# Optimization experiments

Measured on AMD Instinct MI355X. Metric: run time of the kernel, lower is better.

## Reference

```python
import jax, jax.numpy as jnp
import numpy as np

N_NODES, N_EDGES, N_GRAPHS = 20000, 320000, 16
F_NODE, F_EDGE, F_GLOB = 64, 32, 16


def seg_mean(x, idx, num):
    # segment average; segments with zero members yield zeros
    s = jax.ops.segment_sum(x, idx, num_segments=num)
    c = jax.ops.segment_sum(jnp.ones((x.shape[0], 1), x.dtype), idx, num_segments=num)
    return s / jnp.maximum(c, 1.0)


def setup_inputs() -> dict:
    key = jax.random.key(0)
    ks = jax.random.split(key, 24)
    s = 0.05
    inp = {
        'node_feats': jax.random.normal(ks[0], (N_NODES, F_NODE), jnp.float32),
        'edge_feats': jax.random.normal(ks[1], (N_EDGES, F_EDGE), jnp.float32),
        'globals_': jax.random.normal(ks[2], (N_GRAPHS, F_GLOB), jnp.float32),
        'We1': jax.random.normal(ks[3], (256, F_EDGE), jnp.float32) * s,
        'be1': jnp.zeros((256,), jnp.float32),
        'Wn1': jax.random.normal(ks[4], (256, F_NODE), jnp.float32) * s,
        'Win1': jax.random.normal(ks[5], (256, 256), jnp.float32) * s,
        'bn1': jnp.zeros((256,), jnp.float32),
        'We2': jax.random.normal(ks[6], (128, 256), jnp.float32) * s,
        'Wg2': jax.random.normal(ks[7], (128, F_GLOB), jnp.float32) * s,
        'be2': jnp.zeros((128,), jnp.float32),
        'Wn2': jax.random.normal(ks[8], (128, 256), jnp.float32) * s,
        'Win2': jax.random.normal(ks[9], (128, 128), jnp.float32) * s,
        'Wng2': jax.random.normal(ks[10], (128, F_GLOB), jnp.float32) * s,
        'bn2': jnp.zeros((128,), jnp.float32),
        'Wgn': jax.random.normal(ks[11], (128, 128), jnp.float32) * s,
        'Wge': jax.random.normal(ks[12], (128, 128), jnp.float32) * s,
        'Wgg': jax.random.normal(ks[13], (128, F_GLOB), jnp.float32) * s,
        'bg': jnp.zeros((128,), jnp.float32),
        'receivers': jax.random.randint(ks[14], (N_EDGES,), 0, N_NODES, jnp.int32),
        'node_graph': jnp.sort(jax.random.randint(ks[15], (N_NODES,), 0, N_GRAPHS, jnp.int32)),
    }
    return inp


def reference(node_feats, edge_feats, globals_, We1, be1, Wn1, Win1, bn1,
              We2, Wg2, be2, Wn2, Win2, Wng2, bn2, Wgn, Wge, Wgg, bg,
              receivers, node_graph):
    N = node_feats.shape[0]
    B = globals_.shape[0]
    edge_graph = node_graph[receivers]  # graph id of each edge [E]

    # edge1 + relu: e -> 256
    e1 = jax.nn.relu(edge_feats @ We1.T + be1)  # [E,256]
    # node1 + relu: node + avg incoming edges -> 256
    agg1 = seg_mean(e1, receivers, N)  # [N,256]
    n1 = jax.nn.relu(node_feats @ Wn1.T + agg1 @ Win1.T + bn1)  # [N,256]
    # edge2 + relu: edge + broadcast globals -> 128
    e2 = jax.nn.relu(e1 @ We2.T + globals_[edge_graph] @ Wg2.T + be2)  # [E,128]
    # node2 + relu: node + avg incoming edges + broadcast globals -> 128
    agg2 = seg_mean(e2, receivers, N)  # [N,128]
    n2 = jax.nn.relu(n1 @ Wn2.T + agg2 @ Win2.T + globals_[node_graph] @ Wng2.T + bn2)  # [N,128]
    # global: avg nodes + avg edges per graph + globals -> output
    node_avg = seg_mean(n2, node_graph, B)  # [B,128]
    edge_avg = seg_mean(e2, edge_graph, B)  # [B,128]
    out = node_avg @ Wgn.T + edge_avg @ Wge.T + globals_ @ Wgg.T + bg  # [B,128]
    return out
```

## Files before the change

### kernel.cpp

```cpp
#include <hip/hip_runtime.h>
#include <hip/hip_bf16.h>

#define N_NODES 20000
#define N_EDGES 320000
#define NG 16

using bf16 = __hip_bfloat16;
typedef __attribute__((ext_vector_type(8))) short short8v;
typedef __attribute__((ext_vector_type(4))) short short4v;
typedef __attribute__((ext_vector_type(4))) float f32x4;

static __device__ __forceinline__ short f2bs(float f) {
  bf16 h = __float2bfloat16(f);
  union { bf16 b; short s; } u;
  u.b = h;
  return u.s;
}
static __device__ __forceinline__ float bs2f(short s) {
  union { short s; bf16 b; } u;
  u.s = s;
  return __bfloat162float(u.b);
}

__global__ __launch_bounds__(256) void k_prep(
    const float* __restrict__ globals_, const float* __restrict__ Wg2,
    const float* __restrict__ Wng2, const float* __restrict__ Wgg,
    const float* __restrict__ bg, float* __restrict__ g2e,
    float* __restrict__ g2n, float* __restrict__ gg,
    const float* __restrict__ We1, const float* __restrict__ Wn1,
    const float* __restrict__ Win1, const float* __restrict__ We2,
    const float* __restrict__ Wn2, const float* __restrict__ Win2,
    bf16* __restrict__ Wb_e1, bf16* __restrict__ Wb_n1,
    bf16* __restrict__ Wb_e2, bf16* __restrict__ Wb_n2,
    const float* __restrict__ nf, bf16* __restrict__ nfb) {
  int idx = blockIdx.x * 256 + threadIdx.x;
  if (idx < 6144) {
    int arr = idx >> 11;
    int rem = idx & 2047;
    int g = rem >> 7, c = rem & 127;
    const float* W = arr == 0 ? Wg2 : (arr == 1 ? Wng2 : Wgg);
    float acc = (arr == 2) ? bg[c] : 0.f;
#pragma unroll
    for (int k = 0; k < 16; ++k) acc += globals_[g * 16 + k] * W[c * 16 + k];
    float* o = arr == 0 ? g2e : (arr == 1 ? g2n : gg);
    o[rem] = acc;
    return;
  }
  idx -= 6144;
  if (idx < 172032) {
    int i = idx;
    float v;
    bf16* dst;
    int di;
    if (i < 8192) {
      v = We1[i]; dst = Wb_e1; di = i;
    } else if (i < 90112) {
      int j = i - 8192, r = j / 320, c = j % 320;
      v = c < 64 ? Wn1[r * 64 + c] : Win1[r * 256 + (c - 64)];
      dst = Wb_n1; di = j;
    } else if (i < 122880) {
      int j = i - 90112;
      int n = j >> 8, p = j & 255;
      int k = ((p & 15) << 4) | (p >> 4);
      v = We2[n * 256 + k];
      dst = Wb_e2; di = j;
    } else {
      int j = i - 122880, r = j / 384, c = j % 384;
      if (c < 256) {
        int k = ((c & 15) << 4) | (c >> 4);
        v = Wn2[r * 256 + k];
      } else {
        v = Win2[r * 128 + (c - 256)];
      }
      dst = Wb_n2; di = j;
    }
    dst[di] = __float2bfloat16(v);
    return;
  }
  idx -= 172032;
  if (idx < 320000) {
    int n = idx >> 4, q = idx & 15;
    float4 v = *(const float4*)(nf + (size_t)n * 64 + q * 4);
    short4v o = {f2bs(v.x), f2bs(v.y), f2bs(v.z), f2bs(v.w)};
    *(short4v*)((short*)nfb + (size_t)n * 64 + q * 4) = o;
  }
}

__global__ __launch_bounds__(256) void k_counts(
    const int* __restrict__ recv, const int* __restrict__ node_graph,
    int* __restrict__ cnt_node, int* __restrict__ node_cnt_g,
    int* __restrict__ edge_cnt_g) {
  __shared__ int le[NG], ln[NG];
  int tid = threadIdx.x;
  if (tid < NG) { le[tid] = 0; ln[tid] = 0; }
  __syncthreads();
  int idx = blockIdx.x * 256 + tid;
  if (idx < N_EDGES) {
    int r = recv[idx];
    atomicAdd(&cnt_node[r], 1);
    atomicAdd(&le[node_graph[r]], 1);
  } else if (idx < N_EDGES + N_NODES) {
    int n = idx - N_EDGES;
    atomicAdd(&ln[node_graph[n]], 1);
  }
  __syncthreads();
  if (tid < NG && le[tid]) atomicAdd(&edge_cnt_g[tid], le[tid]);
  if (tid >= NG && tid < 2 * NG && ln[tid - NG]) atomicAdd(&node_cnt_g[tid - NG], ln[tid - NG]);
}

__global__ __launch_bounds__(256) void k_scan(const int* __restrict__ cnt,
                                              int* __restrict__ offset,
                                              int* __restrict__ cursor) {
  __shared__ int wsum[4];
  __shared__ int carry_s;
  int tid = threadIdx.x, lane = tid & 63, wv = tid >> 6;
  if (tid == 0) carry_s = 0;
  __syncthreads();
  for (int base = 0; base < N_NODES; base += 1024) {
    int idx = base + tid * 4;
    int v[4];
    int s = 0;
#pragma unroll
    for (int i = 0; i < 4; ++i) {
      v[i] = (idx + i < N_NODES) ? cnt[idx + i] : 0;
      s += v[i];
    }
    int ps = s;
#pragma unroll
    for (int d = 1; d < 64; d <<= 1) {
      int t = __shfl_up(ps, d, 64);
      if (lane >= d) ps += t;
    }
    if (lane == 63) wsum[wv] = ps;
    __syncthreads();
    int wbase = carry_s;
    for (int w2 = 0; w2 < wv; ++w2) wbase += wsum[w2];
    int run = wbase + ps - s;
#pragma unroll
    for (int i = 0; i < 4; ++i) {
      if (idx + i < N_NODES) {
        offset[idx + i] = run;
        cursor[idx + i] = 0;
      }
      run += v[i];
    }
    __syncthreads();
    if (tid == 0) carry_s += wsum[0] + wsum[1] + wsum[2] + wsum[3];
    __syncthreads();
  }
  if (tid == 0) offset[N_NODES] = carry_s;
}

__global__ __launch_bounds__(256) void k_scatter(
    const int* __restrict__ recv, const int* __restrict__ offset,
    int* __restrict__ cursor, int* __restrict__ pos2edge,
    int* __restrict__ pos2node) {
  int e = blockIdx.x * 256 + threadIdx.x;
  if (e >= N_EDGES) return;
  int n = recv[e];
  int slot = atomicAdd(&cursor[n], 1);
  int pos = offset[n] + slot;
  pos2edge[pos] = e;
  pos2node[pos] = n;
}

__global__ __launch_bounds__(256, 4) void k_edge(
    const float* __restrict__ edge_feats, const bf16* __restrict__ We1b,
    const bf16* __restrict__ We2b, const float* __restrict__ be1,
    const float* __restrict__ be2, const float* __restrict__ g2e,
    const int* __restrict__ pos2edge, const int* __restrict__ pos2node,
    const int* __restrict__ node_graph, const int* __restrict__ offset,
    float* __restrict__ agg1f, float* __restrict__ agg2f) {
  __shared__ __align__(16) short t16[64 * 264];
  __shared__ int rownode_s[64];
  __shared__ int rowgid_s[64];
  char* tb = (char*)t16;
  const int tid = threadIdx.x;
  const int wave = tid >> 6, lane = tid & 63;
  const int l15 = lane & 15, grp = lane >> 4;
  const int p0 = blockIdx.x * 64;
  const int base = wave * 16;

  if (tid < 64) {
    int rn = pos2node[p0 + tid];
    rownode_s[tid] = rn;
    rowgid_s[tid] = node_graph[rn];
  }
  const int n0w = tid >> 3, cgw = tid & 7;
  short8v wreg[4];
#pragma unroll
  for (int s = 0; s < 4; ++s)
    wreg[s] = *(const short8v*)((const short*)We2b + (size_t)(n0w + s * 32) * 256 + cgw * 8);
#pragma unroll
  for (int s = 0; s < 4; ++s) {
    int slot = tid + s * 256;
    int n = slot >> 2, cg = slot & 3;
    short8v w8 = *(const short8v*)((const short*)We1b + n * 32 + cg * 8);
    *(short8v*)(tb + n * 64 + ((cg * 16) ^ (((n >> 1) & 3) << 4))) = w8;
  }
  int e = pos2edge[p0 + base + l15];
  const float* efrow = edge_feats + (size_t)e * 32 + grp * 8;
  float4 af0 = *(const float4*)(efrow);
  float4 af1 = *(const float4*)(efrow + 4);
  short8v a1;
  a1[0] = f2bs(af0.x); a1[1] = f2bs(af0.y); a1[2] = f2bs(af0.z); a1[3] = f2bs(af0.w);
  a1[4] = f2bs(af1.x); a1[5] = f2bs(af1.y); a1[6] = f2bs(af1.z); a1[7] = f2bs(af1.w);
  __syncthreads();

  f32x4 acc1[16] = {};
#pragma unroll
  for (int nf = 0; nf < 16; ++nf) {
    int n = nf * 16 + l15;
    short8v b8 = *(const short8v*)(tb + n * 64 + ((grp * 16) ^ (((n >> 1) & 3) << 4)));
    acc1[nf] = __builtin_amdgcn_mfma_f32_16x16x32_bf16(a1, b8, acc1[nf], 0, 0, 0);
  }
#pragma unroll
  for (int nf = 0; nf < 16; ++nf) {
    float bv = be1[nf * 16 + l15];
#pragma unroll
    for (int i = 0; i < 4; ++i) {
      float v = acc1[nf][i] + bv;
      acc1[nf][i] = v > 0.f ? v : 0.f;
    }
  }
  __syncthreads();

#pragma unroll
  for (int i = 0; i < 4; ++i) {
    int row = base + grp * 4 + i;
    short8v lo, hi;
#pragma unroll
    for (int q = 0; q < 8; ++q) {
      lo[q] = f2bs(acc1[q][i]);
      hi[q] = f2bs(acc1[q + 8][i]);
    }
    *(short8v*)&t16[row * 264 + l15 * 16] = lo;
    *(short8v*)&t16[row * 264 + l15 * 16 + 8] = hi;
  }
  __syncthreads();

  bool bnd = (lane == 63) || (rownode_s[lane + 1] != rownode_s[lane]);
  unsigned long long fmask = __ballot(bnd);
  unsigned long long amask = 0;
  {
    unsigned long long lsb = fmask & (~fmask + 1ull);
    if (offset[rownode_s[0]] < p0) amask |= lsb;
    if (offset[rownode_s[63] + 1] > p0 + 64) amask |= 1ull << 63;
  }

  short8v a2[8];
  const short* myrow = &t16[(base + l15) * 264];
#pragma unroll
  for (int s = 0; s < 8; ++s)
    a2[s] = *(const short8v*)(myrow + s * 32 + grp * 8);

  {
    int col = ((tid & 15) << 4) | (tid >> 4);
    float run = 0.f;
#pragma unroll
    for (int rb = 0; rb < 64; rb += 16) {
      float v[16];
#pragma unroll
      for (int i = 0; i < 16; ++i) v[i] = bs2f(t16[(rb + i) * 264 + tid]);
#pragma unroll
      for (int i = 0; i < 16; ++i) {
        run += v[i];
        int r = rb + i;
        if ((fmask >> r) & 1) {
          float* dst = &agg1f[(size_t)rownode_s[r] * 256 + col];
          if ((amask >> r) & 1) atomicAdd(dst, run);
          else *dst = run;
          run = 0.f;
        }
      }
    }
  }
  __syncthreads();

#pragma unroll
  for (int s = 0; s < 4; ++s) {
    int n = n0w + s * 32;
    *(short8v*)(tb + n * 128 + ((cgw * 16) ^ ((n & 7) << 4))) = wreg[s];
  }
#pragma unroll
  for (int s = 0; s < 4; ++s)
    wreg[s] = *(const short8v*)((const short*)We2b + (size_t)(n0w + s * 32) * 256 + 64 + cgw * 8);
  __syncthreads();

  f32x4 acc2[8] = {};
#pragma unroll
  for (int c = 0; c < 4; ++c) {
    const int bufo = (c & 1) ? 16384 : 0;
    if (c < 3) {
      const int nbufo = ((c + 1) & 1) ? 16384 : 0;
#pragma unroll
      for (int s = 0; s < 4; ++s) {
        int n = n0w + s * 32;
        *(short8v*)(tb + nbufo + n * 128 + ((cgw * 16) ^ ((n & 7) << 4))) = wreg[s];
      }
      if (c < 2) {
#pragma unroll
        for (int s = 0; s < 4; ++s)
          wreg[s] = *(const short8v*)((const short*)We2b +
                                      (size_t)(n0w + s * 32) * 256 + (c + 2) * 64 + cgw * 8);
      }
    }
#pragma unroll
    for (int kki = 0; kki < 2; ++kki) {
#pragma unroll
      for (int nf = 0; nf < 8; ++nf) {
        int n = nf * 16 + l15;
        short8v b8 = *(const short8v*)(tb + bufo + n * 128 +
                                       (((kki * 64) + grp * 16) ^ ((n & 7) << 4)));
        acc2[nf] = __builtin_amdgcn_mfma_f32_16x16x32_bf16(a2[c * 2 + kki], b8,
                                                           acc2[nf], 0, 0, 0);
      }
    }
    if (c < 3) __syncthreads();
  }

  int gidr[4];
#pragma unroll
  for (int i = 0; i < 4; ++i) gidr[i] = rowgid_s[base + grp * 4 + i];
#pragma unroll
  for (int nf = 0; nf < 8; ++nf) {
    int col = nf * 16 + l15;
    float bv = be2[col];
#pragma unroll
    for (int i = 0; i < 4; ++i) {
      float v = acc2[nf][i] + bv + g2e[gidr[i] * 128 + col];
      acc2[nf][i] = v > 0.f ? v : 0.f;
    }
  }
  __syncthreads();

  float* tf32 = (float*)t16;
#pragma unroll
  for (int i = 0; i < 4; ++i) {
    int row = base + grp * 4 + i;
    float4 lo = {acc2[0][i], acc2[1][i], acc2[2][i], acc2[3][i]};
    float4 hi = {acc2[4][i], acc2[5][i], acc2[6][i], acc2[7][i]};
    *(float4*)&tf32[row * 132 + l15 * 8] = lo;
    *(float4*)&tf32[row * 132 + l15 * 8 + 4] = hi;
  }
  __syncthreads();

  if (tid < 128) {
    int col = ((tid & 7) << 4) | (tid >> 3);
    float run = 0.f;
#pragma unroll
    for (int rb = 0; rb < 64; rb += 16) {
      float v[16];
#pragma unroll
      for (int i = 0; i < 16; ++i) v[i] = tf32[(rb + i) * 132 + tid];
#pragma unroll
      for (int i = 0; i < 16; ++i) {
        run += v[i];
        int r = rb + i;
        if ((fmask >> r) & 1) {
          float* dst = &agg2f[(size_t)rownode_s[r] * 128 + col];
          if ((amask >> r) & 1) atomicAdd(dst, run);
          else *dst = run;
          run = 0.f;
        }
      }
    }
  }
}

__global__ __launch_bounds__(256, 2) void k_node(
    const bf16* __restrict__ nfb, const float* __restrict__ agg1f,
    const float* __restrict__ agg2f, const int* __restrict__ offset,
    const bf16* __restrict__ Wn1b, const bf16* __restrict__ Wn2b,
    const float* __restrict__ bn1, const float* __restrict__ bn2,
    const float* __restrict__ g2n, const int* __restrict__ node_graph,
    float* __restrict__ node_sum, float* __restrict__ edge_sum) {
  __shared__ __align__(16) char smem_w[32768];
  __shared__ __align__(16) short t16[64 * 264];
  __shared__ int rowgid_s[64];
  const int tid = threadIdx.x;
  const int wave = tid >> 6, lane = tid & 63;
  const int l15 = lane & 15, grp = lane >> 4;
  const int r0 = blockIdx.x * 64;
  const int base = wave * 16;
  const int n0w = tid >> 3, cgw = tid & 7;

  if (tid < 64) {
    int n = r0 + tid;
    rowgid_s[tid] = node_graph[n < N_NODES ? n : N_NODES - 1];
  }
  long arow = r0 + base + l15;
  if (arow >= N_NODES) arow = N_NODES - 1;
  int dg = offset[arow + 1] - offset[arow];
  const float inv = 1.f / (float)(dg > 1 ? dg : 1);

  short8v a1all[10];
#pragma unroll
  for (int kki = 0; kki < 2; ++kki)
    a1all[kki] = *(const short8v*)((const short*)nfb + (size_t)arow * 64 + kki * 32 + grp * 8);
#pragma unroll
  for (int c = 1; c < 5; ++c) {
#pragma unroll
    for (int kki = 0; kki < 2; ++kki) {
      int k = c * 64 + kki * 32 + grp * 8;
      const float* p = agg1f + (size_t)arow * 256 + (k - 64);
      float4 f0 = *(const float4*)p;
      float4 f1 = *(const float4*)(p + 4);
      short8v t;
      t[0] = f2bs(f0.x * inv); t[1] = f2bs(f0.y * inv);
      t[2] = f2bs(f0.z * inv); t[3] = f2bs(f0.w * inv);
      t[4] = f2bs(f1.x * inv); t[5] = f2bs(f1.y * inv);
      t[6] = f2bs(f1.z * inv); t[7] = f2bs(f1.w * inv);
      a1all[c * 2 + kki] = t;
    }
  }

  short8v w1x[8], w1y[8];
#pragma unroll
  for (int s = 0; s < 8; ++s)
    w1x[s] = *(const short8v*)((const short*)Wn1b + (size_t)(n0w + s * 32) * 320 + cgw * 8);
#pragma unroll
  for (int s = 0; s < 8; ++s)
    w1y[s] = *(const short8v*)((const short*)Wn1b + (size_t)(n0w + s * 32) * 320 + 64 + cgw * 8);
  f32x4 acc1[16] = {};
#pragma unroll
  for (int c = 0; c < 5; ++c) {
    if (c > 0) __syncthreads();
#pragma unroll
    for (int s = 0; s < 8; ++s) {
      int n = n0w + s * 32;
      *(short8v*)(smem_w + n * 128 + ((cgw * 16) ^ ((n & 7) << 4))) =
          (c & 1) ? w1y[s] : w1x[s];
    }
    if (c + 2 < 5) {
#pragma unroll
      for (int s = 0; s < 8; ++s) {
        short8v t = *(const short8v*)((const short*)Wn1b +
                                      (size_t)(n0w + s * 32) * 320 + (c + 2) * 64 + cgw * 8);
        if (c & 1) w1y[s] = t;
        else w1x[s] = t;
      }
    }
    __syncthreads();
#pragma unroll
    for (int kki = 0; kki < 2; ++kki) {
#pragma unroll
      for (int nf = 0; nf < 16; ++nf) {
        int wrow = nf * 16 + l15;
        short8v b8 = *(const short8v*)(smem_w + wrow * 128 +
                                       (((kki * 64) + grp * 16) ^ ((wrow & 7) << 4)));
        acc1[nf] = __builtin_amdgcn_mfma_f32_16x16x32_bf16(a1all[c * 2 + kki], b8,
                                                           acc1[nf], 0, 0, 0);
      }
    }
  }

#pragma unroll
  for (int nf = 0; nf < 16; ++nf) {
    float bv = bn1[nf * 16 + l15];
#pragma unroll
    for (int i = 0; i < 4; ++i) {
      float v = acc1[nf][i] + bv;
      acc1[nf][i] = v > 0.f ? v : 0.f;
    }
  }
#pragma unroll
  for (int i = 0; i < 4; ++i) {
    int row = base + grp * 4 + i;
    short8v lo, hi;
#pragma unroll
    for (int q = 0; q < 8; ++q) {
      lo[q] = f2bs(acc1[q][i]);
      hi[q] = f2bs(acc1[q + 8][i]);
    }
    *(short8v*)&t16[row * 264 + l15 * 16] = lo;
    *(short8v*)&t16[row * 264 + l15 * 16 + 8] = hi;
  }
  short8v a2all[12];
  const short* myrow = &t16[(base + l15) * 264];
#pragma unroll
  for (int s = 0; s < 8; ++s)
    a2all[s] = *(const short8v*)(myrow + s * 32 + grp * 8);
#pragma unroll
  for (int c = 4; c < 6; ++c) {
#pragma unroll
    for (int kki = 0; kki < 2; ++kki) {
      int k = (c - 4) * 64 + kki * 32 + grp * 8;
      const float* p = agg2f + (size_t)arow * 128 + k;
      float4 f0 = *(const float4*)p;
      float4 f1 = *(const float4*)(p + 4);
      short8v t;
      t[0] = f2bs(f0.x * inv); t[1] = f2bs(f0.y * inv);
      t[2] = f2bs(f0.z * inv); t[3] = f2bs(f0.w * inv);
      t[4] = f2bs(f1.x * inv); t[5] = f2bs(f1.y * inv);
      t[6] = f2bs(f1.z * inv); t[7] = f2bs(f1.w * inv);
      a2all[c * 2 + kki] = t;
    }
  }
  short8v w2r[24];
#pragma unroll
  for (int c = 0; c < 6; ++c)
#pragma unroll
    for (int s = 0; s < 4; ++s)
      w2r[c * 4 + s] = *(const short8v*)((const short*)Wn2b +
                                         (size_t)(n0w + s * 32) * 384 + c * 64 + cgw * 8);

  f32x4 acc2[8] = {};
#pragma unroll
  for (int c = 0; c < 6; ++c) {
    __syncthreads();
#pragma unroll
    for (int s = 0; s < 4; ++s) {
      int n = n0w + s * 32;
      *(short8v*)(smem_w + n * 128 + ((cgw * 16) ^ ((n & 7) << 4))) = w2r[c * 4 + s];
    }
    __syncthreads();
#pragma unroll
    for (int kki = 0; kki < 2; ++kki) {
#pragma unroll
      for (int nf = 0; nf < 8; ++nf) {
        int wrow = nf * 16 + l15;
        short8v b8 = *(const short8v*)(smem_w + wrow * 128 +
                                       (((kki * 64) + grp * 16) ^ ((wrow & 7) << 4)));
        acc2[nf] = __builtin_amdgcn_mfma_f32_16x16x32_bf16(a2all[c * 2 + kki], b8,
                                                           acc2[nf], 0, 0, 0);
      }
    }
  }

  float* tf32 = (float*)t16;
  int gidr[4];
#pragma unroll
  for (int i = 0; i < 4; ++i) gidr[i] = rowgid_s[base + grp * 4 + i];
#pragma unroll
  for (int nf = 0; nf < 8; ++nf) {
    int col = nf * 16 + l15;
    float bv = bn2[col];
#pragma unroll
    for (int i = 0; i < 4; ++i) {
      float v = acc2[nf][i] + bv + g2n[gidr[i] * 128 + col];
      acc2[nf][i] = v > 0.f ? v : 0.f;
    }
  }
#pragma unroll
  for (int i = 0; i < 4; ++i) {
    int row = base + grp * 4 + i;
    float4 lo = {acc2[0][i], acc2[1][i], acc2[2][i], acc2[3][i]};
    float4 hi = {acc2[4][i], acc2[5][i], acc2[6][i], acc2[7][i]};
    *(float4*)&tf32[row * 132 + l15 * 8] = lo;
    *(float4*)&tf32[row * 132 + l15 * 8 + 4] = hi;
  }
  __syncthreads();

  bool gb = (lane == 63) || (rowgid_s[lane + 1] != rowgid_s[lane]);
  unsigned long long gmask = __ballot(gb);
  if (tid < 128) {
    int col = ((tid & 7) << 4) | (tid >> 3);
    float rn_ = 0.f, re_ = 0.f;
#pragma unroll
    for (int rb = 0; rb < 64; rb += 16) {
      float vn[16], ve[16];
#pragma unroll
      for (int i = 0; i < 16; ++i) {
        int r = rb + i;
        long row = (long)r0 + r;
        bool ok = row < N_NODES;
        vn[i] = ok ? tf32[r * 132 + tid] : 0.f;
        ve[i] = ok ? agg2f[(size_t)row * 128 + col] : 0.f;
      }
#pragma unroll
      for (int i = 0; i < 16; ++i) {
        int r = rb + i;
        rn_ += vn[i];
        re_ += ve[i];
        if ((gmask >> r) & 1) {
          int g = rowgid_s[r];
          atomicAdd(&node_sum[g * 128 + col], rn_);
          atomicAdd(&edge_sum[g * 128 + col], re_);
          rn_ = 0.f;
          re_ = 0.f;
        }
      }
    }
  }
}

__global__ __launch_bounds__(128) void k_final(
    const float* __restrict__ node_sum, const float* __restrict__ edge_sum,
    const int* __restrict__ node_cnt_g, const int* __restrict__ edge_cnt_g,
    const float* __restrict__ Wgn, const float* __restrict__ Wge,
    const float* __restrict__ gg, float* __restrict__ out) {
  __shared__ float navg[128], eavg[128];
  const int g = blockIdx.x, c = threadIdx.x;
  int nc = node_cnt_g[g];
  nc = nc > 1 ? nc : 1;
  int ec = edge_cnt_g[g];
  ec = ec > 1 ? ec : 1;
  navg[c] = node_sum[g * 128 + c] / (float)nc;
  eavg[c] = edge_sum[g * 128 + c] / (float)ec;
  __syncthreads();
  float acc = gg[g * 128 + c];
#pragma unroll 4
  for (int k = 0; k < 128; ++k)
    acc += navg[k] * Wgn[c * 128 + k] + eavg[k] * Wge[c * 128 + k];
  out[g * 128 + c] = acc;
}

extern "C" void kernel_launch(void* const* d_in, const int* in_sizes, int n_in,
                              void* d_out, int out_size, void* d_ws, size_t ws_size,
                              hipStream_t stream) {
  const float* node_feats = (const float*)d_in[0];
  const float* edge_feats = (const float*)d_in[1];
  const float* globals_ = (const float*)d_in[2];
  const float* We1 = (const float*)d_in[3];
  const float* be1 = (const float*)d_in[4];
  const float* Wn1 = (const float*)d_in[5];
  const float* Win1 = (const float*)d_in[6];
  const float* bn1 = (const float*)d_in[7];
  const float* We2 = (const float*)d_in[8];
  const float* Wg2 = (const float*)d_in[9];
  const float* be2 = (const float*)d_in[10];
  const float* Wn2 = (const float*)d_in[11];
  const float* Win2 = (const float*)d_in[12];
  const float* Wng2 = (const float*)d_in[13];
  const float* bn2 = (const float*)d_in[14];
  const float* Wgn = (const float*)d_in[15];
  const float* Wge = (const float*)d_in[16];
  const float* Wgg = (const float*)d_in[17];
  const float* bg = (const float*)d_in[18];
  const int* receivers = (const int*)d_in[19];
  const int* node_graph = (const int*)d_in[20];
  float* out = (float*)d_out;

  char* ws = (char*)d_ws;
  size_t off = 0;
  auto alloc = [&](size_t bytes) {
    size_t o = off;
    off += (bytes + 255) & ~(size_t)255;
    return o;
  };
  const int NP = 20032;
  int* cnt_node = (int*)(ws + alloc((size_t)N_NODES * 4));
  int* node_cnt_g = (int*)(ws + alloc(NG * 4));
  int* edge_cnt_g = (int*)(ws + alloc(NG * 4));
  float* node_sum = (float*)(ws + alloc(NG * 128 * 4));
  float* edge_sum = (float*)(ws + alloc(NG * 128 * 4));
  float* agg1f = (float*)(ws + alloc((size_t)N_NODES * 256 * 4));
  float* agg2f = (float*)(ws + alloc((size_t)N_NODES * 128 * 4));
  size_t zero_bytes = off;
  int* offset = (int*)(ws + alloc((size_t)(N_NODES + 1) * 4));
  int* cursor = (int*)(ws + alloc((size_t)N_NODES * 4));
  int* pos2edge = (int*)(ws + alloc((size_t)N_EDGES * 4));
  int* pos2node = (int*)(ws + alloc((size_t)N_EDGES * 4));
  float* g2e = (float*)(ws + alloc(NG * 128 * 4));
  float* g2n = (float*)(ws + alloc(NG * 128 * 4));
  float* gg = (float*)(ws + alloc(NG * 128 * 4));
  bf16* Wb_e1 = (bf16*)(ws + alloc(8192 * 2));
  bf16* Wb_n1 = (bf16*)(ws + alloc(81920 * 2));
  bf16* Wb_e2 = (bf16*)(ws + alloc(32768 * 2));
  bf16* Wb_n2 = (bf16*)(ws + alloc(49152 * 2));
  bf16* nfb = (bf16*)(ws + alloc((size_t)NP * 64 * 2));
  (void)ws_size;

  hipMemsetAsync(d_ws, 0, zero_bytes, stream);
  k_prep<<<1946, 256, 0, stream>>>(globals_, Wg2, Wng2, Wgg, bg, g2e, g2n, gg,
                                   We1, Wn1, Win1, We2, Wn2, Win2, Wb_e1,
                                   Wb_n1, Wb_e2, Wb_n2, node_feats, nfb);
  k_counts<<<(N_EDGES + N_NODES + 255) / 256, 256, 0, stream>>>(
      receivers, node_graph, cnt_node, node_cnt_g, edge_cnt_g);
  k_scan<<<1, 256, 0, stream>>>(cnt_node, offset, cursor);
  k_scatter<<<(N_EDGES + 255) / 256, 256, 0, stream>>>(receivers, offset,
                                                       cursor, pos2edge,
                                                       pos2node);
  k_edge<<<N_EDGES / 64, 256, 0, stream>>>(edge_feats, Wb_e1, Wb_e2, be1, be2,
                                           g2e, pos2edge, pos2node, node_graph,
                                           offset, agg1f, agg2f);
  k_node<<<NP / 64, 256, 0, stream>>>(nfb, agg1f, agg2f, offset, Wb_n1, Wb_n2,
                                      bn1, bn2, g2n, node_graph, node_sum,
                                      edge_sum);
  k_final<<<NG, 128, 0, stream>>>(node_sum, edge_sum, node_cnt_g, edge_cnt_g,
                                  Wgn, Wge, gg, out);
}
```

Baseline: 195.7 us.

## Make edge kernel persistent over five tiles with prefetch of next tile

The edge kernel now launches 1000 blocks that each process five 64-edge tiles in a loop instead of one tile per block. While the current tile is being reduced into agg1f, each block prefetches the next tile's edge features, node ids and graph ids, and it also reloads the first We2 chunk for the next iteration. The aim is to hide global load latency and amortize per-block setup. The cost is fewer blocks in flight (1000 blocks on a large GPU), extra register pressure, and the We1 tile being restaged into shared memory on every iteration.

```diff
diff --git a/kernel.cpp b/kernel.cpp
--- a/kernel.cpp
+++ b/kernel.cpp
@@ -172,199 +172,243 @@
     const int* __restrict__ node_graph, const int* __restrict__ offset,
     float* __restrict__ agg1f, float* __restrict__ agg2f) {
   __shared__ __align__(16) short t16[64 * 264];
-  __shared__ int rownode_s[64];
-  __shared__ int rowgid_s[64];
+  __shared__ int rownode_s[2][64];
+  __shared__ int rowgid_s[2][64];
   char* tb = (char*)t16;
   const int tid = threadIdx.x;
   const int wave = tid >> 6, lane = tid & 63;
   const int l15 = lane & 15, grp = lane >> 4;
-  const int p0 = blockIdx.x * 64;
   const int base = wave * 16;
-
-  if (tid < 64) {
-    int rn = pos2node[p0 + tid];
-    rownode_s[tid] = rn;
-    rowgid_s[tid] = node_graph[rn];
-  }
   const int n0w = tid >> 3, cgw = tid & 7;
+
+  int rn_next = 0, rg_next = 0;
+  short8v a1_next;
   short8v wreg[4];
-#pragma unroll
-  for (int s = 0; s < 4; ++s)
-    wreg[s] = *(const short8v*)((const short*)We2b + (size_t)(n0w + s * 32) * 256 + cgw * 8);
-#pragma unroll
-  for (int s = 0; s < 4; ++s) {
-    int slot = tid + s * 256;
-    int n = slot >> 2, cg = slot & 3;
-    short8v w8 = *(const short8v*)((const short*)We1b + n * 32 + cg * 8);
-    *(short8v*)(tb + n * 64 + ((cg * 16) ^ (((n >> 1) & 3) << 4))) = w8;
-  }
-  int e = pos2edge[p0 + base + l15];
-  const float* efrow = edge_feats + (size_t)e * 32 + grp * 8;
-  float4 af0 = *(const float4*)(efrow);
-  float4 af1 = *(const float4*)(efrow + 4);
-  short8v a1;
-  a1[0] = f2bs(af0.x); a1[1] = f2bs(af0.y); a1[2] = f2bs(af0.z); a1[3] = f2bs(af0.w);
-  a1[4] = f2bs(af1.x); a1[5] = f2bs(af1.y); a1[6] = f2bs(af1.z); a1[7] = f2bs(af1.w);
-  __syncthreads();
-
-  f32x4 acc1[16] = {};
-#pragma unroll
-  for (int nf = 0; nf < 16; ++nf) {
-    int n = nf * 16 + l15;
-    short8v b8 = *(const short8v*)(tb + n * 64 + ((grp * 16) ^ (((n >> 1) & 3) << 4)));
-    acc1[nf] = __builtin_amdgcn_mfma_f32_16x16x32_bf16(a1, b8, acc1[nf], 0, 0, 0);
-  }
-#pragma unroll
-  for (int nf = 0; nf < 16; ++nf) {
-    float bv = be1[nf * 16 + l15];
+  {
+    const int tile0 = blockIdx.x * 5;
+    if (tid < 64) {
+      rn_next = pos2node[tile0 * 64 + tid];
+      rg_next = node_graph[rn_next];
+    }
+    int e0 = pos2edge[tile0 * 64 + base + l15];
+    const float* er = edge_feats + (size_t)e0 * 32 + grp * 8;
+    float4 a = *(const float4*)er;
+    float4 b = *(const float4*)(er + 4);
+    a1_next[0] = f2bs(a.x); a1_next[1] = f2bs(a.y);
+    a1_next[2] = f2bs(a.z); a1_next[3] = f2bs(a.w);
+    a1_next[4] = f2bs(b.x); a1_next[5] = f2bs(b.y);
+    a1_next[6] = f2bs(b.z); a1_next[7] = f2bs(b.w);
+#pragma unroll
+    for (int s = 0; s < 4; ++s)
+      wreg[s] = *(const short8v*)((const short*)We2b + (size_t)(n0w + s * 32) * 256 + cgw * 8);
+  }
+
+#pragma unroll 1
+  for (int t = 0; t < 5; ++t) {
+    const int tile = blockIdx.x * 5 + t;
+    const int p0 = tile * 64;
+    const int pr = t & 1;
+    __syncthreads();
+    if (tid < 64) {
+      rownode_s[pr][tid] = rn_next;
+      rowgid_s[pr][tid] = rg_next;
+    }
+#pragma unroll
+    for (int s = 0; s < 4; ++s) {
+      int slot = tid + s * 256;
+      int n = slot >> 2, cg = slot & 3;
+      short8v w8 = *(const short8v*)((const short*)We1b + n * 32 + cg * 8);
+      *(short8v*)(tb + n * 64 + ((cg * 16) ^ (((n >> 1) & 3) << 4))) = w8;
+    }
+    short8v a1 = a1_next;
+    __syncthreads();
+
+    f32x4 acc1[16] = {};
+#pragma unroll
+    for (int nf = 0; nf < 16; ++nf) {
+      int n = nf * 16 + l15;
+      short8v b8 = *(const short8v*)(tb + n * 64 + ((grp * 16) ^ (((n >> 1) & 3) << 4)));
+      acc1[nf] = __builtin_amdgcn_mfma_f32_16x16x32_bf16(a1, b8, acc1[nf], 0, 0, 0);
+    }
+#pragma unroll
+    for (int nf = 0; nf < 16; ++nf) {
+      float bv = be1[nf * 16 + l15];
+#pragma unroll
+      for (int i = 0; i < 4; ++i) {
+        float v = acc1[nf][i] + bv;
+        acc1[nf][i] = v > 0.f ? v : 0.f;
+      }
+    }
+    __syncthreads();
+
 #pragma unroll
     for (int i = 0; i < 4; ++i) {
-      float v = acc1[nf][i] + bv;
-      acc1[nf][i] = v > 0.f ? v : 0.f;
-    }
-  }
-  __syncthreads();
-
-#pragma unroll
-  for (int i = 0; i < 4; ++i) {
-    int row = base + grp * 4 + i;
-    short8v lo, hi;
-#pragma unroll
-    for (int q = 0; q < 8; ++q) {
-      lo[q] = f2bs(acc1[q][i]);
-      hi[q] = f2bs(acc1[q + 8][i]);
-    }
-    *(short8v*)&t16[row * 264 + l15 * 16] = lo;
-    *(short8v*)&t16[row * 264 + l15 * 16 + 8] = hi;
-  }
-  __syncthreads();
-
-  bool bnd = (lane == 63) || (rownode_s[lane + 1] != rownode_s[lane]);
-  unsigned long long fmask = __ballot(bnd);
-  unsigned long long amask = 0;
-  {
-    unsigned long long lsb = fmask & (~fmask + 1ull);
-    if (offset[rownode_s[0]] < p0) amask |= lsb;
-    if (offset[rownode_s[63] + 1] > p0 + 64) amask |= 1ull << 63;
-  }
-
-  short8v a2[8];
-  const short* myrow = &t16[(base + l15) * 264];
-#pragma unroll
-  for (int s = 0; s < 8; ++s)
-    a2[s] = *(const short8v*)(myrow + s * 32 + grp * 8);
-
-  {
-    int col = ((tid & 15) << 4) | (tid >> 4);
-    float run = 0.f;
-#pragma unroll
-    for (int rb = 0; rb < 64; rb += 16) {
-      float v[16];
-#pragma unroll
-      for (int i = 0; i < 16; ++i) v[i] = bs2f(t16[(rb + i) * 264 + tid]);
-#pragma unroll
-      for (int i = 0; i < 16; ++i) {
-        run += v[i];
-        int r = rb + i;
-        if ((fmask >> r) & 1) {
-          float* dst = &agg1f[(size_t)rownode_s[r] * 256 + col];
-          if ((amask >> r) & 1) atomicAdd(dst, run);
-          else *dst = run;
-          run = 0.f;
+      int row = base + grp * 4 + i;
+      short8v lo, hi;
+#pragma unroll
+      for (int q = 0; q < 8; ++q) {
+        lo[q] = f2bs(acc1[q][i]);
+        hi[q] = f2bs(acc1[q + 8][i]);
+      }
+      *(short8v*)&t16[row * 264 + l15 * 16] = lo;
+      *(short8v*)&t16[row * 264 + l15 * 16 + 8] = hi;
+    }
+    __syncthreads();
+
+    bool bnd = (lane == 63) || (rownode_s[pr][lane + 1] != rownode_s[pr][lane]);
+    unsigned long long fmask = __ballot(bnd);
+    unsigned long long amask = 0;
+    {
+      unsigned long long lsb = fmask & (~fmask + 1ull);
+      if (offset[rownode_s[pr][0]] < p0) amask |= lsb;
+      if (offset[rownode_s[pr][63] + 1] > p0 + 64) amask |= 1ull << 63;
+    }
+
+    short8v a2[8];
+    const short* myrow = &t16[(base + l15) * 264];
+#pragma unroll
+    for (int s = 0; s < 8; ++s)
+      a2[s] = *(const short8v*)(myrow + s * 32 + grp * 8);
+
+    int rnN = 0, rgN = 0;
+    short8v a1N;
+    {
+      const int tilen = blockIdx.x * 5 + ((t < 4) ? t + 1 : t);
+      if (tid < 64) {
+        rnN = pos2node[tilen * 64 + tid];
+        rgN = node_graph[rnN];
+      }
+      int eN = pos2edge[tilen * 64 + base + l15];
+      const float* erN = edge_feats + (size_t)eN * 32 + grp * 8;
+      float4 aN = *(const float4*)erN;
+      float4 bN = *(const float4*)(erN + 4);
+      a1N[0] = f2bs(aN.x); a1N[1] = f2bs(aN.y);
+      a1N[2] = f2bs(aN.z); a1N[3] = f2bs(aN.w);
+      a1N[4] = f2bs(bN.x); a1N[5] = f2bs(bN.y);
+      a1N[6] = f2bs(bN.z); a1N[7] = f2bs(bN.w);
+    }
+
+    {
+      int col = ((tid & 15) << 4) | (tid >> 4);
+      float run = 0.f;
+#pragma unroll
+      for (int rb = 0; rb < 64; rb += 16) {
+        float v[16];
+#pragma unroll
+        for (int i = 0; i < 16; ++i) v[i] = bs2f(t16[(rb + i) * 264 + tid]);
+#pragma unroll
+        for (int i = 0; i < 16; ++i) {
+          run += v[i];
+          int r = rb + i;
+          if ((fmask >> r) & 1) {
+            float* dst = &agg1f[(size_t)rownode_s[pr][r] * 256 + col];
+            if ((amask >> r) & 1) atomicAdd(dst, run);
+            else *dst = run;
+            run = 0.f;
+          }
         }
       }
     }
-  }
-  __syncthreads();
-
-#pragma unroll
-  for (int s = 0; s < 4; ++s) {
-    int n = n0w + s * 32;
-    *(short8v*)(tb + n * 128 + ((cgw * 16) ^ ((n & 7) << 4))) = wreg[s];
-  }
-#pragma unroll
-  for (int s = 0; s < 4; ++s)
-    wreg[s] = *(const short8v*)((const short*)We2b + (size_t)(n0w + s * 32) * 256 + 64 + cgw * 8);
-  __syncthreads();
-
-  f32x4 acc2[8] = {};
-#pragma unroll
-  for (int c = 0; c < 4; ++c) {
-    const int bufo = (c & 1) ? 16384 : 0;
-    if (c < 3) {
-      const int nbufo = ((c + 1) & 1) ? 16384 : 0;
-#pragma unroll
-      for (int s = 0; s < 4; ++s) {
-        int n = n0w + s * 32;
-        *(short8v*)(tb + nbufo + n * 128 + ((cgw * 16) ^ ((n & 7) << 4))) = wreg[s];
-      }
-      if (c < 2) {
-#pragma unroll
-        for (int s = 0; s < 4; ++s)
-          wreg[s] = *(const short8v*)((const short*)We2b +
-                                      (size_t)(n0w + s * 32) * 256 + (c + 2) * 64 + cgw * 8);
-      }
-    }
-#pragma unroll
-    for (int kki = 0; kki < 2; ++kki) {
-#pragma unroll
-      for (int nf = 0; nf < 8; ++nf) {
-        int n = nf * 16 + l15;
-        short8v b8 = *(const short8v*)(tb + bufo + n * 128 +
-                                       (((kki * 64) + grp * 16) ^ ((n & 7) << 4)));
-        acc2[nf] = __builtin_amdgcn_mfma_f32_16x16x32_bf16(a2[c * 2 + kki], b8,
-                                                           acc2[nf], 0, 0, 0);
-      }
-    }
-    if (c < 3) __syncthreads();
-  }
-
-  int gidr[4];
-#pragma unroll
-  for (int i = 0; i < 4; ++i) gidr[i] = rowgid_s[base + grp * 4 + i];
-#pragma unroll
-  for (int nf = 0; nf < 8; ++nf) {
-    int col = nf * 16 + l15;
-    float bv = be2[col];
+    __syncthreads();
+
+#pragma unroll
+    for (int s = 0; s < 4; ++s) {
+      int n = n0w + s * 32;
+      *(short8v*)(tb + n * 128 + ((cgw * 16) ^ ((n & 7) << 4))) = wreg[s];
+    }
+#pragma unroll
+    for (int s = 0; s < 4; ++s)
+      wreg[s] = *(const short8v*)((const short*)We2b +
+                                  (size_t)(n0w + s * 32) * 256 + 64 + cgw * 8);
+    __syncthreads();
+
+    f32x4 acc2[8] = {};
+#pragma unroll
+    for (int c = 0; c < 4; ++c) {
+      const int bufo = (c & 1) ? 16384 : 0;
+      if (c < 3) {
+        const int nbufo = ((c + 1) & 1) ? 16384 : 0;
+#pragma unroll
+        for (int s = 0; s < 4; ++s) {
+          int n = n0w + s * 32;
+          *(short8v*)(tb + nbufo + n * 128 + ((cgw * 16) ^ ((n & 7) << 4))) = wreg[s];
+        }
+        if (c < 2) {
+#pragma unroll
+          for (int s = 0; s < 4; ++s)
+            wreg[s] = *(const short8v*)((const short*)We2b +
+                                        (size_t)(n0w + s * 32) * 256 + (c + 2) * 64 + cgw * 8);
+        } else {
+#pragma unroll
+          for (int s = 0; s < 4; ++s)
+            wreg[s] = *(const short8v*)((const short*)We2b +
+                                        (size_t)(n0w + s * 32) * 256 + cgw * 8);
+        }
+      }
+#pragma unroll
+      for (int kki = 0; kki < 2; ++kki) {
+#pragma unroll
+        for (int nf = 0; nf < 8; ++nf) {
+          int n = nf * 16 + l15;
+          short8v b8 = *(const short8v*)(tb + bufo + n * 128 +
+                                         (((kki * 64) + grp * 16) ^ ((n & 7) << 4)));
+          acc2[nf] = __builtin_amdgcn_mfma_f32_16x16x32_bf16(a2[c * 2 + kki], b8,
+                                                             acc2[nf], 0, 0, 0);
+        }
+      }
+      if (c < 3) __syncthreads();
+    }
+
+    int gidr[4];
+#pragma unroll
+    for (int i = 0; i < 4; ++i) gidr[i] = rowgid_s[pr][base + grp * 4 + i];
+#pragma unroll
+    for (int nf = 0; nf < 8; ++nf) {
+      int col = nf * 16 + l15;
+      float bv = be2[col];
+#pragma unroll
+      for (int i = 0; i < 4; ++i) {
+        float v = acc2[nf][i] + bv + g2e[gidr[i] * 128 + col];
+        acc2[nf][i] = v > 0.f ? v : 0.f;
+      }
+    }
+    __syncthreads();
+
+    float* tf32 = (float*)t16;
 #pragma unroll
     for (int i = 0; i < 4; ++i) {
-      float v = acc2[nf][i] + bv + g2e[gidr[i] * 128 + col];
-      acc2[nf][i] = v > 0.f ? v : 0.f;
-    }
-  }
-  __syncthreads();
-
-  float* tf32 = (float*)t16;
-#pragma unroll
-  for (int i = 0; i < 4; ++i) {
-    int row = base + grp * 4 + i;
-    float4 lo = {acc2[0][i], acc2[1][i], acc2[2][i], acc2[3][i]};
-    float4 hi = {acc2[4][i], acc2[5][i], acc2[6][i], acc2[7][i]};
-    *(float4*)&tf32[row * 132 + l15 * 8] = lo;
-    *(float4*)&tf32[row * 132 + l15 * 8 + 4] = hi;
-  }
-  __syncthreads();
-
-  if (tid < 128) {
-    int col = ((tid & 7) << 4) | (tid >> 3);
-    float run = 0.f;
-#pragma unroll
-    for (int rb = 0; rb < 64; rb += 16) {
-      float v[16];
-#pragma unroll
-      for (int i = 0; i < 16; ++i) v[i] = tf32[(rb + i) * 132 + tid];
-#pragma unroll
-      for (int i = 0; i < 16; ++i) {
-        run += v[i];
-        int r = rb + i;
-        if ((fmask >> r) & 1) {
-          float* dst = &agg2f[(size_t)rownode_s[r] * 128 + col];
-          if ((amask >> r) & 1) atomicAdd(dst, run);
-          else *dst = run;
-          run = 0.f;
+      int row = base + grp * 4 + i;
+      float4 lo = {acc2[0][i], acc2[1][i], acc2[2][i], acc2[3][i]};
+      float4 hi = {acc2[4][i], acc2[5][i], acc2[6][i], acc2[7][i]};
+      *(float4*)&tf32[row * 132 + l15 * 8] = lo;
+      *(float4*)&tf32[row * 132 + l15 * 8 + 4] = hi;
+    }
+    __syncthreads();
+
+    if (tid < 128) {
+      int col = ((tid & 7) << 4) | (tid >> 3);
+      float run = 0.f;
+#pragma unroll
+      for (int rb = 0; rb < 64; rb += 16) {
+        float v[16];
+#pragma unroll
+        for (int i = 0; i < 16; ++i) v[i] = tf32[(rb + i) * 132 + tid];
+#pragma unroll
+        for (int i = 0; i < 16; ++i) {
+          run += v[i];
+          int r = rb + i;
+          if ((fmask >> r) & 1) {
+            float* dst = &agg2f[(size_t)rownode_s[pr][r] * 128 + col];
+            if ((amask >> r) & 1) atomicAdd(dst, run);
+            else *dst = run;
+            run = 0.f;
+          }
         }
       }
     }
+    rn_next = rnN;
+    rg_next = rgN;
+    a1_next = a1N;
   }
 }
 
@@ -672,9 +716,9 @@
   k_scatter<<<(N_EDGES + 255) / 256, 256, 0, stream>>>(receivers, offset,
                                                        cursor, pos2edge,
                                                        pos2node);
-  k_edge<<<N_EDGES / 64, 256, 0, stream>>>(edge_feats, Wb_e1, Wb_e2, be1, be2,
-                                           g2e, pos2edge, pos2node, node_graph,
-                                           offset, agg1f, agg2f);
+  k_edge<<<1000, 256, 0, stream>>>(edge_feats, Wb_e1, Wb_e2, be1, be2,
+                                   g2e, pos2edge, pos2node, node_graph,
+                                   offset, agg1f, agg2f);
   k_node<<<NP / 64, 256, 0, stream>>>(nfb, agg1f, agg2f, offset, Wb_n1, Wb_n2,
                                       bn1, bn2, g2n, node_graph, node_sum,
                                       edge_sum);
```

Measured after the change: 239.4 us. +22.3%, slower.
